# Kernel optimization log

Measured on AMD Instinct MI355X. Metric: run time of the kernel, lower is better.

Reference implementation:

```python
import jax, jax.numpy as jnp
import numpy as np

N_NODES = 100000
N_EDGES = 1600000
N_GRAPHS = 200
NODES_PER_GRAPH = N_NODES // N_GRAPHS
IN_DIM, HID, LAT = 24, 64, 32


def setup_inputs() -> dict:
    key = jax.random.key(0)
    ks = jax.random.split(key, 12)
    x = jax.random.normal(ks[0], (N_NODES, IN_DIM), jnp.float32)
    edge_index = jax.random.randint(ks[1], (2, N_EDGES), 0, N_NODES, jnp.int32)
    batch = (jnp.arange(N_NODES, dtype=jnp.int32) // NODES_PER_GRAPH)
    eps = jax.random.normal(ks[2], (N_GRAPHS, LAT), jnp.float32)

    def lin(k, i, o):
        s = 1.0 / np.sqrt(i)
        return jax.random.uniform(k, (i, o), jnp.float32, -s, s)

    return {
        "x": x, "edge_index": edge_index, "batch": batch, "eps": eps,
        "W1": lin(ks[3], IN_DIM, HID), "b1": jnp.zeros((HID,), jnp.float32),
        "W2": lin(ks[4], HID, HID), "b2": jnp.zeros((HID,), jnp.float32),
        "Wmu": lin(ks[5], HID, LAT), "bmu": jnp.zeros((LAT,), jnp.float32),
        "Wlv": lin(ks[6], HID, LAT), "blv": jnp.zeros((LAT,), jnp.float32),
        "Wd1": lin(ks[7], LAT, 128), "bd1": jnp.zeros((128,), jnp.float32),
        "Wd2": lin(ks[8], 128, IN_DIM), "bd2": jnp.zeros((IN_DIM,), jnp.float32),
        "num_nodes_per_graph": NODES_PER_GRAPH,
        "num_graphs": N_GRAPHS,
    }


def gcn_conv(x, edge_index, W, b, n_nodes):
    # PyG GCNConv: linear transform, add self-loops, symmetric normalization,
    # scatter-add aggregation at target (col) nodes, then bias.
    h = x @ W  # [N, out]
    loops = jnp.arange(n_nodes, dtype=edge_index.dtype)
    row = jnp.concatenate([edge_index[0], loops])  # source nodes
    col = jnp.concatenate([edge_index[1], loops])  # target nodes
    deg = jax.ops.segment_sum(jnp.ones_like(col, h.dtype), col, n_nodes)
    dinv = jnp.where(deg > 0, jax.lax.rsqrt(deg), 0.0)
    norm = dinv[row] * dinv[col]  # [E+N]
    msg = h[row] * norm[:, None]  # gather + scale (memory-bound)
    out = jax.ops.segment_sum(msg, col, n_nodes)  # scatter-add
    return out + b


def reference(x, edge_index, batch, eps, W1, b1, W2, b2, Wmu, bmu, Wlv, blv,
              Wd1, bd1, Wd2, bd2, num_nodes_per_graph, num_graphs):
    n_nodes = x.shape[0]
    h = jax.nn.relu(gcn_conv(x, edge_index, W1, b1, n_nodes))
    h = jax.nn.relu(gcn_conv(h, edge_index, W2, b2, n_nodes))
    # global mean pool over graphs
    sums = jax.ops.segment_sum(h, batch, num_graphs)
    cnt = jax.ops.segment_sum(jnp.ones((n_nodes,), h.dtype), batch, num_graphs)
    pooled = sums / jnp.maximum(cnt, 1.0)[:, None]
    mu = pooled @ Wmu + bmu
    logvar = pooled @ Wlv + blv
    # reparameterize with provided eps (torch.randn_like surrogate)
    z = mu + eps * jnp.exp(0.5 * logvar)
    # decoder: repeat each z num_nodes_per_graph times
    z_exp = jnp.repeat(z, num_nodes_per_graph, axis=0)  # [G*nn, LAT]
    hd = jax.nn.relu(z_exp @ Wd1 + bd1)
    recon_x = jax.nn.sigmoid(hd @ Wd2 + bd2)
    return recon_x, mu, logvar
```

## Files before the change

kernel.cpp:

```cpp
#include <hip/hip_runtime.h>
#include <hip/hip_bf16.h>
#include <hip/hip_fp8.h>

constexpr int N_NODES = 100000;
constexpr int N_EDGES = 1600000;
constexpr int N_GRAPHS = 200;
constexpr int NPG = 500;
constexpr int IN_DIM = 24;
constexpr int HID = 64;
constexpr int LAT = 32;
constexpr int DEC = 128;
constexpr int CAP = 48;
constexpr int P2 = 512;
constexpr int NPP = 196;
constexpr int PART_CAP = 3840;
constexpr int KP_BLOCKS = 200;
constexpr int KP_CHUNK = N_EDGES / KP_BLOCKS;

typedef __attribute__((ext_vector_type(8))) short short8;
typedef __attribute__((ext_vector_type(4))) float f32x4;
typedef __attribute__((ext_vector_type(2))) float f32x2;

constexpr int OFF_CNT = 0;
constexpr int OFF_GCOUNT = 100000;
constexpr int OFF_ROWS = 102400;
constexpr int OFF_A = OFF_ROWS + N_NODES * CAP;
constexpr int OFF_B = OFF_A + N_NODES * HID / 2;
constexpr int OFF_HS1 = OFF_B + N_NODES * HID / 2;
constexpr int OFF_PARTIAL = OFF_HS1 + (N_NODES + 1) * 16;

__global__ __launch_bounds__(1024) void k_part(const int* __restrict__ ei,
                                               int* __restrict__ gcount,
                                               unsigned int* __restrict__ epart) {
    __shared__ int hist[P2];
    __shared__ int ptrs[P2];
    int t = threadIdx.x;
    for (int i = t; i < P2; i += 1024) hist[i] = 0;
    __syncthreads();
    int e0 = blockIdx.x * KP_CHUNK;
    const int4* cols4 = reinterpret_cast<const int4*>(ei + N_EDGES + e0);
    const int4* rows4 = reinterpret_cast<const int4*>(ei + e0);
    for (int i = t; i < KP_CHUNK / 4; i += 1024) {
        int4 c = cols4[i];
        atomicAdd(&hist[c.x / NPP], 1);
        atomicAdd(&hist[c.y / NPP], 1);
        atomicAdd(&hist[c.z / NPP], 1);
        atomicAdd(&hist[c.w / NPP], 1);
    }
    __syncthreads();
    for (int i = t; i < P2; i += 1024) ptrs[i] = atomicAdd(gcount + i, hist[i]);
    __syncthreads();
    for (int i = t; i < KP_CHUNK / 4; i += 1024) {
        int4 c = cols4[i];
        int4 r = rows4[i];
#pragma unroll
        for (int k = 0; k < 4; ++k) {
            int cc = (k == 0) ? c.x : (k == 1) ? c.y : (k == 2) ? c.z : c.w;
            int rr = (k == 0) ? r.x : (k == 1) ? r.y : (k == 2) ? r.z : r.w;
            int p = cc / NPP;
            int cl = cc - p * NPP;
            int pos = atomicAdd(&ptrs[p], 1);
            if (pos < PART_CAP)
                epart[p * PART_CAP + pos] = ((unsigned)cl << 17) | (unsigned)rr;
        }
    }
}

__device__ inline unsigned char f2fp8(float f) {
    __hip_fp8_e4m3 v(f);
    return (unsigned char)v.__x;
}

__device__ inline unsigned short f2bf(float f) {
    __hip_bfloat16 h = __float2bfloat16(f);
    return *reinterpret_cast<unsigned short*>(&h);
}

__global__ __launch_bounds__(256) void k_fill3_lin1(
    const unsigned int* __restrict__ epart, const int* __restrict__ gcount,
    const float* __restrict__ x, const float* __restrict__ W1,
    int* __restrict__ cnt, int* __restrict__ rows,
    unsigned char* __restrict__ HS1) {
    __shared__ int lcnt[NPP];
    __shared__ int lrows[NPP * CAP];
    __shared__ float Ws[IN_DIM * HID];
    int p = blockIdx.x, t = threadIdx.x;
    if (p == 0 && t < 16)
        reinterpret_cast<unsigned int*>(HS1)[N_NODES * 16 + t] = 0;
    for (int i = t; i < NPP; i += 256) lcnt[i] = 0;
    for (int i = t; i < IN_DIM * HID; i += 256) Ws[i] = W1[i];
    __syncthreads();
    int m = min(gcount[p], PART_CAP);
    for (int i = t; i < m; i += 256) {
        unsigned v = epart[p * PART_CAP + i];
        int cl = v >> 17;
        int r = (int)(v & 0x1FFFFu);
        int pos = atomicAdd(&lcnt[cl], 1);
        if (pos < CAP) lrows[cl * CAP + pos] = r;
    }
    __syncthreads();
    for (int i = t; i < NPP; i += 256) {
        int c = min(lcnt[i], CAP);
        int cp = min((c + 3) & ~3, CAP);
        for (int j = c; j < cp; ++j) lrows[i * CAP + j] = N_NODES;
    }
    __syncthreads();
    int node0 = p * NPP;
    int nn = min(NPP, N_NODES - node0);
    if (nn <= 0) return;
    for (int i = t; i < nn * CAP; i += 256) rows[node0 * CAP + i] = lrows[i];
    for (int i = t; i < nn; i += 256) cnt[node0 + i] = lcnt[i];
    __syncthreads();
    float* xs = reinterpret_cast<float*>(lrows);
    for (int i = t; i < nn * IN_DIM; i += 256) xs[i] = x[node0 * IN_DIM + i];
    __syncthreads();
    for (int o = t; o < nn * HID; o += 256) {
        int j = o >> 6, col = o & 63;
        float acc = 0.f;
#pragma unroll
        for (int k = 0; k < IN_DIM; ++k) acc += xs[j * IN_DIM + k] * Ws[k * HID + col];
        float dinv = rsqrtf((float)(lcnt[j] + 1));
        HS1[(node0 + j) * HID + col] = f2fp8(acc * dinv);
    }
}

__device__ inline void acc_fp8x4p(unsigned int u, f32x2& lo, f32x2& hi) {
    lo += __builtin_amdgcn_cvt_pk_f32_fp8(u, false);
    hi += __builtin_amdgcn_cvt_pk_f32_fp8(u, true);
}

__device__ inline void fold4(float4& a) {
    a.x += __shfl_xor(a.x, 16, 64); a.x += __shfl_xor(a.x, 32, 64);
    a.y += __shfl_xor(a.y, 16, 64); a.y += __shfl_xor(a.y, 32, 64);
    a.z += __shfl_xor(a.z, 16, 64); a.z += __shfl_xor(a.z, 32, 64);
    a.w += __shfl_xor(a.w, 16, 64); a.w += __shfl_xor(a.w, 32, 64);
}

__device__ inline void gather_quad(int base, int lane, int np0, int np1,
                                   int np2, int np3,
                                   const int* __restrict__ rows,
                                   const unsigned char* __restrict__ HS,
                                   float4& A0, float4& A1, float4& A2, float4& A3) {
    int fq = lane & 15;
    int rs = lane >> 4;
    const unsigned int* HSq = reinterpret_cast<const unsigned int*>(HS);
    const int* rb = rows + base * CAP;
    int idx0 = (lane < np0) ? rb[lane] : 0;
    int idx1 = (lane < np1) ? rb[CAP + lane] : 0;
    int idx2 = (lane < np2) ? rb[2 * CAP + lane] : 0;
    int idx3 = (lane < np3) ? rb[3 * CAP + lane] : 0;
    f32x2 z = {0.f, 0.f};
    f32x2 l0 = z, h0 = z, l1 = z, h1 = z, l2 = z, h2 = z, l3 = z, h3 = z;
    if (rs == 0)      acc_fp8x4p(HSq[(base + 0) * 16 + fq], l0, h0);
    else if (rs == 1) acc_fp8x4p(HSq[(base + 1) * 16 + fq], l1, h1);
    else if (rs == 2) acc_fp8x4p(HSq[(base + 2) * 16 + fq], l2, h2);
    else              acc_fp8x4p(HSq[(base + 3) * 16 + fq], l3, h3);
    int nw0 = np0 >> 2, nw1 = np1 >> 2, nw2 = np2 >> 2, nw3 = np3 >> 2;
    int gmax = max(max(nw0, nw1), max(nw2, nw3));
    for (int g = 0; g < gmax; g += 4) {
        int m0 = nw0 - g, m1 = nw1 - g, m2 = nw2 - g, m3 = nw3 - g;
        unsigned int u0[4], u1[4], u2[4], u3[4];
#pragma unroll
        for (int k = 0; k < 4; ++k) {
            int sl = 4 * (g + k) + rs;
            if (k < m0) { int r = __shfl(idx0, sl, 64); u0[k] = HSq[r * 16 + fq]; }
            if (k < m1) { int r = __shfl(idx1, sl, 64); u1[k] = HSq[r * 16 + fq]; }
            if (k < m2) { int r = __shfl(idx2, sl, 64); u2[k] = HSq[r * 16 + fq]; }
            if (k < m3) { int r = __shfl(idx3, sl, 64); u3[k] = HSq[r * 16 + fq]; }
        }
#pragma unroll
        for (int k = 0; k < 4; ++k) {
            if (k < m0) acc_fp8x4p(u0[k], l0, h0);
            if (k < m1) acc_fp8x4p(u1[k], l1, h1);
            if (k < m2) acc_fp8x4p(u2[k], l2, h2);
            if (k < m3) acc_fp8x4p(u3[k], l3, h3);
        }
    }
    float4 a0 = {l0.x, l0.y, h0.x, h0.y};
    float4 a1 = {l1.x, l1.y, h1.x, h1.y};
    float4 a2 = {l2.x, l2.y, h2.x, h2.y};
    float4 a3 = {l3.x, l3.y, h3.x, h3.y};
    fold4(a0); fold4(a1); fold4(a2); fold4(a3);
    A0 = a0; A1 = a1; A2 = a2; A3 = a3;
}

__global__ __launch_bounds__(256) void k_gather1(const int* __restrict__ cnt,
                                                 const int* __restrict__ rows,
                                                 const unsigned char* __restrict__ HS1,
                                                 const float* __restrict__ b1,
                                                 unsigned short* __restrict__ H1) {
    int tid = threadIdx.x;
    int w = (blockIdx.x * 256 + tid) >> 6;
    int lane = tid & 63;
    int base = w * 4;
    int cn0 = cnt[base], cn1 = cnt[base + 1], cn2 = cnt[base + 2], cn3 = cnt[base + 3];
    int np0 = (min(cn0, CAP) + 3) & ~3;
    int np1 = (min(cn1, CAP) + 3) & ~3;
    int np2 = (min(cn2, CAP) + 3) & ~3;
    int np3 = (min(cn3, CAP) + 3) & ~3;
    float4 a0, a1, a2, a3;
    gather_quad(base, lane, np0, np1, np2, np3, rows, HS1, a0, a1, a2, a3);
    int fq = lane & 15, rs = lane >> 4;
    float4 bv = reinterpret_cast<const float4*>(b1)[fq];
    float4 a = (rs == 0) ? a0 : (rs == 1) ? a1 : (rs == 2) ? a2 : a3;
    int cn = (rs == 0) ? cn0 : (rs == 1) ? cn1 : (rs == 2) ? cn2 : cn3;
    float dinv = rsqrtf((float)(cn + 1));
    ushort4 o;
    o.x = f2bf(fmaxf(dinv * a.x + bv.x, 0.f));
    o.y = f2bf(fmaxf(dinv * a.y + bv.y, 0.f));
    o.z = f2bf(fmaxf(dinv * a.z + bv.z, 0.f));
    o.w = f2bf(fmaxf(dinv * a.w + bv.w, 0.f));
    *reinterpret_cast<ushort4*>(H1 + (base + rs) * HID + 4 * fq) = o;
}

__global__ __launch_bounds__(256) void k_gemm2(const unsigned short* __restrict__ H1,
                                               const float* __restrict__ W2,
                                               const int* __restrict__ cnt,
                                               unsigned char* __restrict__ HS2) {
    __shared__ unsigned short W2T[HID * 72];
    int tid = threadIdx.x;
    if (blockIdx.x == 0 && tid < 16)
        reinterpret_cast<unsigned int*>(HS2)[N_NODES * 16 + tid] = 0;
    for (int i = tid; i < HID * HID; i += 256) {
        int k = i >> 6, n = i & 63;
        W2T[n * 72 + k] = f2bf(W2[i]);
    }
    __syncthreads();
    int wave = tid >> 6, lane = tid & 63;
    int wid = blockIdx.x * 4 + wave;
    if (wid >= N_NODES / 16) return;
    int row0 = wid * 16;
    int m = lane & 15, quad = lane >> 4;
    const short8* Av = reinterpret_cast<const short8*>(H1);
    short8 a0 = Av[(row0 + m) * 8 + quad];
    short8 a1 = Av[(row0 + m) * 8 + 4 + quad];
    float dv[4];
#pragma unroll
    for (int reg = 0; reg < 4; ++reg)
        dv[reg] = rsqrtf((float)(cnt[row0 + quad * 4 + reg] + 1));
#pragma unroll
    for (int nt = 0; nt < 4; ++nt) {
        short8 b0 = *reinterpret_cast<const short8*>(&W2T[(nt * 16 + m) * 72 + quad * 8]);
        short8 b1 = *reinterpret_cast<const short8*>(&W2T[(nt * 16 + m) * 72 + 32 + quad * 8]);
        f32x4 acc = {0.f, 0.f, 0.f, 0.f};
        acc = __builtin_amdgcn_mfma_f32_16x16x32_bf16(a0, b0, acc, 0, 0, 0);
        acc = __builtin_amdgcn_mfma_f32_16x16x32_bf16(a1, b1, acc, 0, 0, 0);
#pragma unroll
        for (int reg = 0; reg < 4; ++reg) {
            int r = row0 + quad * 4 + reg;
            HS2[r * HID + nt * 16 + m] = f2fp8(acc[reg] * dv[reg]);
        }
    }
}

__global__ __launch_bounds__(256) void k_gather2(const int* __restrict__ cnt,
                                                 const int* __restrict__ rows,
                                                 const unsigned char* __restrict__ HS2,
                                                 const float* __restrict__ b2,
                                                 float* __restrict__ partial) {
    int tid = threadIdx.x;
    int w = (blockIdx.x * 256 + tid) >> 6;
    int lane = tid & 63;
    int base = w * 4;
    int cn0 = cnt[base], cn1 = cnt[base + 1], cn2 = cnt[base + 2], cn3 = cnt[base + 3];
    int np0 = (min(cn0, CAP) + 3) & ~3;
    int np1 = (min(cn1, CAP) + 3) & ~3;
    int np2 = (min(cn2, CAP) + 3) & ~3;
    int np3 = (min(cn3, CAP) + 3) & ~3;
    float4 a0, a1, a2, a3;
    gather_quad(base, lane, np0, np1, np2, np3, rows, HS2, a0, a1, a2, a3);
    int fq = lane & 15, rs = lane >> 4;
    float4 bv = reinterpret_cast<const float4*>(b2)[fq];
    float d0 = rsqrtf((float)(cn0 + 1));
    float d1 = rsqrtf((float)(cn1 + 1));
    float d2 = rsqrtf((float)(cn2 + 1));
    float d3 = rsqrtf((float)(cn3 + 1));
    float4 s;
    s.x = fmaxf(d0 * a0.x + bv.x, 0.f) + fmaxf(d1 * a1.x + bv.x, 0.f) +
          fmaxf(d2 * a2.x + bv.x, 0.f) + fmaxf(d3 * a3.x + bv.x, 0.f);
    s.y = fmaxf(d0 * a0.y + bv.y, 0.f) + fmaxf(d1 * a1.y + bv.y, 0.f) +
          fmaxf(d2 * a2.y + bv.y, 0.f) + fmaxf(d3 * a3.y + bv.y, 0.f);
    s.z = fmaxf(d0 * a0.z + bv.z, 0.f) + fmaxf(d1 * a1.z + bv.z, 0.f) +
          fmaxf(d2 * a2.z + bv.z, 0.f) + fmaxf(d3 * a3.z + bv.z, 0.f);
    s.w = fmaxf(d0 * a0.w + bv.w, 0.f) + fmaxf(d1 * a1.w + bv.w, 0.f) +
          fmaxf(d2 * a2.w + bv.w, 0.f) + fmaxf(d3 * a3.w + bv.w, 0.f);
    if (rs == 0) reinterpret_cast<float4*>(partial + w * HID)[fq] = s;
}

__global__ __launch_bounds__(128) void k_head_bcast(
    const float* __restrict__ partial, const float* __restrict__ eps,
    const float* __restrict__ Wmu, const float* __restrict__ bmu,
    const float* __restrict__ Wlv, const float* __restrict__ blv,
    const float* __restrict__ Wd1, const float* __restrict__ bd1,
    const float* __restrict__ Wd2, const float* __restrict__ bd2,
    float* __restrict__ out_mu, float* __restrict__ out_lv,
    float* __restrict__ out_recon) {
    int g = blockIdx.x, tid = threadIdx.x;
    __shared__ float p[HID];
    __shared__ float zs[LAT];
    __shared__ float hds[DEC];
    __shared__ __align__(16) float rg[IN_DIM];
    if (tid < HID) {
        float s = 0.f;
#pragma unroll 5
        for (int r = 0; r < NPG / 4; ++r)
            s += partial[(g * (NPG / 4) + r) * HID + tid];
        p[tid] = s * (1.0f / NPG);
    }
    __syncthreads();
    if (tid < LAT) {
        float m = bmu[tid], l = blv[tid];
#pragma unroll 8
        for (int k = 0; k < HID; ++k) {
            m += p[k] * Wmu[k * LAT + tid];
            l += p[k] * Wlv[k * LAT + tid];
        }
        out_mu[g * LAT + tid] = m;
        out_lv[g * LAT + tid] = l;
        zs[tid] = m + eps[g * LAT + tid] * expf(0.5f * l);
    }
    __syncthreads();
    {
        float a = bd1[tid];
#pragma unroll 8
        for (int k = 0; k < LAT; ++k) a += zs[k] * Wd1[k * DEC + tid];
        hds[tid] = fmaxf(a, 0.f);
    }
    __syncthreads();
    if (tid < IN_DIM) {
        float a = bd2[tid];
#pragma unroll 8
        for (int k = 0; k < DEC; ++k) a += hds[k] * Wd2[k * IN_DIM + tid];
        rg[tid] = 1.0f / (1.0f + expf(-a));
    }
    __syncthreads();
    const float4* rg4 = reinterpret_cast<const float4*>(rg);
    float4* dst = reinterpret_cast<float4*>(out_recon + g * NPG * IN_DIM);
    for (int j = tid; j < NPG * IN_DIM / 4; j += 128) dst[j] = rg4[j % (IN_DIM / 4)];
}

extern "C" void kernel_launch(void* const* d_in, const int* in_sizes, int n_in,
                              void* d_out, int out_size, void* d_ws, size_t ws_size,
                              hipStream_t stream) {
    const float* x = (const float*)d_in[0];
    const int* ei = (const int*)d_in[1];
    const float* eps = (const float*)d_in[3];
    const float* W1 = (const float*)d_in[4];
    const float* b1 = (const float*)d_in[5];
    const float* W2 = (const float*)d_in[6];
    const float* b2 = (const float*)d_in[7];
    const float* Wmu = (const float*)d_in[8];
    const float* bmu = (const float*)d_in[9];
    const float* Wlv = (const float*)d_in[10];
    const float* blv = (const float*)d_in[11];
    const float* Wd1 = (const float*)d_in[12];
    const float* bd1 = (const float*)d_in[13];
    const float* Wd2 = (const float*)d_in[14];
    const float* bd2 = (const float*)d_in[15];

    float* ws = (float*)d_ws;
    int* cnt = (int*)ws + OFF_CNT;
    int* gcount = (int*)ws + OFF_GCOUNT;
    int* rows = (int*)ws + OFF_ROWS;
    unsigned int* epart = (unsigned int*)((int*)ws + OFF_A);
    unsigned char* HS1 = (unsigned char*)((int*)ws + OFF_HS1);
    unsigned short* H1 = (unsigned short*)((int*)ws + OFF_B);
    unsigned char* HS2 = (unsigned char*)((int*)ws + OFF_A);
    float* partial = ws + OFF_PARTIAL;

    float* out = (float*)d_out;
    float* out_recon = out;
    float* out_mu = out + N_NODES * IN_DIM;
    float* out_lv = out_mu + N_GRAPHS * LAT;

    hipMemsetAsync(gcount, 0, P2 * sizeof(int), stream);

    k_part<<<KP_BLOCKS, 1024, 0, stream>>>(ei, gcount, epart);
    k_fill3_lin1<<<P2, 256, 0, stream>>>(epart, gcount, x, W1, cnt, rows, HS1);

    k_gather1<<<N_NODES / 16, 256, 0, stream>>>(cnt, rows, HS1, b1, H1);
    k_gemm2<<<(N_NODES / 16 + 3) / 4, 256, 0, stream>>>(H1, W2, cnt, HS2);

    k_gather2<<<N_NODES / 16, 256, 0, stream>>>(cnt, rows, HS2, b2, partial);

    k_head_bcast<<<N_GRAPHS, 128, 0, stream>>>(partial, eps, Wmu, bmu, Wlv, blv,
                                               Wd1, bd1, Wd2, bd2, out_mu,
                                               out_lv, out_recon);
}
```

Measured before the change: 246.3 us.

## Fuse layer-1 gather with layer-2 MFMA GEMM and remap gather to node-per-quarter-wave

Merges the layer-1 neighbour gather and the W2 bf16 MFMA transform into one kernel, so H1 is staged in shared memory instead of being written to and re-read from global memory, and one launch is removed. The gather is restructured so that each 16-lane group of a wave handles one node with a fixed unrolled batch of 32 (optionally 48) neighbour loads, with invalid slots pointing at the zero sentinel row. This drops the padding pass in the fill kernel. The fixed unroll trades wasted loads on low-degree nodes for more memory-level parallelism. Every gather block now also converts W2 into shared memory, and nontemporal loads and stores are used for the index and partial data.

Measured after the change: 205.4 us. 1.2x faster.

```diff
diff --git a/kernel.cpp b/kernel.cpp
--- a/kernel.cpp
+++ b/kernel.cpp
@@ -99,12 +99,6 @@
         if (pos < CAP) lrows[cl * CAP + pos] = r;
     }
     __syncthreads();
-    for (int i = t; i < NPP; i += 256) {
-        int c = min(lcnt[i], CAP);
-        int cp = min((c + 3) & ~3, CAP);
-        for (int j = c; j < cp; ++j) lrows[i * CAP + j] = N_NODES;
-    }
-    __syncthreads();
     int node0 = p * NPP;
     int nn = min(NPP, N_NODES - node0);
     if (nn <= 0) return;
@@ -129,95 +123,62 @@
     hi += __builtin_amdgcn_cvt_pk_f32_fp8(u, true);
 }
 
-__device__ inline void fold4(float4& a) {
-    a.x += __shfl_xor(a.x, 16, 64); a.x += __shfl_xor(a.x, 32, 64);
-    a.y += __shfl_xor(a.y, 16, 64); a.y += __shfl_xor(a.y, 32, 64);
-    a.z += __shfl_xor(a.z, 16, 64); a.z += __shfl_xor(a.z, 32, 64);
-    a.w += __shfl_xor(a.w, 16, 64); a.w += __shfl_xor(a.w, 32, 64);
-}
-
-__device__ inline void gather_quad(int base, int lane, int np0, int np1,
-                                   int np2, int np3,
-                                   const int* __restrict__ rows,
-                                   const unsigned char* __restrict__ HS,
-                                   float4& A0, float4& A1, float4& A2, float4& A3) {
-    int fq = lane & 15;
-    int rs = lane >> 4;
+__device__ inline void gatherT(int base, int lane,
+                               const int* __restrict__ cnt,
+                               const int* __restrict__ rows,
+                               const unsigned char* __restrict__ HS,
+                               f32x2& lo, f32x2& hi, int& cn_out) {
+    int fq = lane & 15, rs = lane >> 4;
     const unsigned int* HSq = reinterpret_cast<const unsigned int*>(HS);
-    const int* rb = rows + base * CAP;
-    int idx0 = (lane < np0) ? rb[lane] : 0;
-    int idx1 = (lane < np1) ? rb[CAP + lane] : 0;
-    int idx2 = (lane < np2) ? rb[2 * CAP + lane] : 0;
-    int idx3 = (lane < np3) ? rb[3 * CAP + lane] : 0;
+    int node = base + rs;
+    int cn = __builtin_nontemporal_load(cnt + node);
+    int np = min(cn, CAP);
+    int mx = np;
+    mx = max(mx, __shfl_xor(mx, 16, 64));
+    mx = max(mx, __shfl_xor(mx, 32, 64));
+    const int* rb = rows + node * CAP;
+    int idx0 = (fq < np)      ? __builtin_nontemporal_load(rb + fq)      : N_NODES;
+    int idx1 = (16 + fq < np) ? __builtin_nontemporal_load(rb + 16 + fq) : N_NODES;
+    int idx2 = (32 + fq < np) ? __builtin_nontemporal_load(rb + 32 + fq) : N_NODES;
     f32x2 z = {0.f, 0.f};
-    f32x2 l0 = z, h0 = z, l1 = z, h1 = z, l2 = z, h2 = z, l3 = z, h3 = z;
-    if (rs == 0)      acc_fp8x4p(HSq[(base + 0) * 16 + fq], l0, h0);
-    else if (rs == 1) acc_fp8x4p(HSq[(base + 1) * 16 + fq], l1, h1);
-    else if (rs == 2) acc_fp8x4p(HSq[(base + 2) * 16 + fq], l2, h2);
-    else              acc_fp8x4p(HSq[(base + 3) * 16 + fq], l3, h3);
-    int nw0 = np0 >> 2, nw1 = np1 >> 2, nw2 = np2 >> 2, nw3 = np3 >> 2;
-    int gmax = max(max(nw0, nw1), max(nw2, nw3));
-    for (int g = 0; g < gmax; g += 4) {
-        int m0 = nw0 - g, m1 = nw1 - g, m2 = nw2 - g, m3 = nw3 - g;
-        unsigned int u0[4], u1[4], u2[4], u3[4];
-#pragma unroll
-        for (int k = 0; k < 4; ++k) {
-            int sl = 4 * (g + k) + rs;
-            if (k < m0) { int r = __shfl(idx0, sl, 64); u0[k] = HSq[r * 16 + fq]; }
-            if (k < m1) { int r = __shfl(idx1, sl, 64); u1[k] = HSq[r * 16 + fq]; }
-            if (k < m2) { int r = __shfl(idx2, sl, 64); u2[k] = HSq[r * 16 + fq]; }
-            if (k < m3) { int r = __shfl(idx3, sl, 64); u3[k] = HSq[r * 16 + fq]; }
-        }
-#pragma unroll
-        for (int k = 0; k < 4; ++k) {
-            if (k < m0) acc_fp8x4p(u0[k], l0, h0);
-            if (k < m1) acc_fp8x4p(u1[k], l1, h1);
-            if (k < m2) acc_fp8x4p(u2[k], l2, h2);
-            if (k < m3) acc_fp8x4p(u3[k], l3, h3);
-        }
-    }
-    float4 a0 = {l0.x, l0.y, h0.x, h0.y};
-    float4 a1 = {l1.x, l1.y, h1.x, h1.y};
-    float4 a2 = {l2.x, l2.y, h2.x, h2.y};
-    float4 a3 = {l3.x, l3.y, h3.x, h3.y};
-    fold4(a0); fold4(a1); fold4(a2); fold4(a3);
-    A0 = a0; A1 = a1; A2 = a2; A3 = a3;
-}
-
-__global__ __launch_bounds__(256) void k_gather1(const int* __restrict__ cnt,
-                                                 const int* __restrict__ rows,
-                                                 const unsigned char* __restrict__ HS1,
-                                                 const float* __restrict__ b1,
-                                                 unsigned short* __restrict__ H1) {
-    int tid = threadIdx.x;
-    int w = (blockIdx.x * 256 + tid) >> 6;
-    int lane = tid & 63;
-    int base = w * 4;
-    int cn0 = cnt[base], cn1 = cnt[base + 1], cn2 = cnt[base + 2], cn3 = cnt[base + 3];
-    int np0 = (min(cn0, CAP) + 3) & ~3;
-    int np1 = (min(cn1, CAP) + 3) & ~3;
-    int np2 = (min(cn2, CAP) + 3) & ~3;
-    int np3 = (min(cn3, CAP) + 3) & ~3;
-    float4 a0, a1, a2, a3;
-    gather_quad(base, lane, np0, np1, np2, np3, rows, HS1, a0, a1, a2, a3);
-    int fq = lane & 15, rs = lane >> 4;
-    float4 bv = reinterpret_cast<const float4*>(b1)[fq];
-    float4 a = (rs == 0) ? a0 : (rs == 1) ? a1 : (rs == 2) ? a2 : a3;
-    int cn = (rs == 0) ? cn0 : (rs == 1) ? cn1 : (rs == 2) ? cn2 : cn3;
-    float dinv = rsqrtf((float)(cn + 1));
-    ushort4 o;
-    o.x = f2bf(fmaxf(dinv * a.x + bv.x, 0.f));
-    o.y = f2bf(fmaxf(dinv * a.y + bv.y, 0.f));
-    o.z = f2bf(fmaxf(dinv * a.z + bv.z, 0.f));
-    o.w = f2bf(fmaxf(dinv * a.w + bv.w, 0.f));
-    *reinterpret_cast<ushort4*>(H1 + (base + rs) * HID + 4 * fq) = o;
-}
-
-__global__ __launch_bounds__(256) void k_gemm2(const unsigned short* __restrict__ H1,
-                                               const float* __restrict__ W2,
-                                               const int* __restrict__ cnt,
-                                               unsigned char* __restrict__ HS2) {
+    lo = z; hi = z;
+    acc_fp8x4p(HSq[node * 16 + fq], lo, hi);
+    int rbase = rs * 16;
+    {
+        unsigned int u[32];
+#pragma unroll
+        for (int c = 0; c < 16; ++c) {
+            int r = __shfl(idx0, rbase + c, 64);
+            u[c] = HSq[r * 16 + fq];
+        }
+#pragma unroll
+        for (int c = 0; c < 16; ++c) {
+            int r = __shfl(idx1, rbase + c, 64);
+            u[16 + c] = HSq[r * 16 + fq];
+        }
+#pragma unroll
+        for (int c = 0; c < 32; ++c) acc_fp8x4p(u[c], lo, hi);
+    }
+    if (mx > 32) {
+        unsigned int u[16];
+#pragma unroll
+        for (int c = 0; c < 16; ++c) {
+            int r = __shfl(idx2, rbase + c, 64);
+            u[c] = HSq[r * 16 + fq];
+        }
+#pragma unroll
+        for (int c = 0; c < 16; ++c) acc_fp8x4p(u[c], lo, hi);
+    }
+    cn_out = cn;
+}
+
+__global__ __launch_bounds__(256) void k_gather1mm(
+    const int* __restrict__ cnt, const int* __restrict__ rows,
+    const unsigned char* __restrict__ HS1, const float* __restrict__ b1,
+    const float* __restrict__ W2, unsigned char* __restrict__ HS2) {
     __shared__ unsigned short W2T[HID * 72];
+    __shared__ unsigned short H1s[16 * 72];
+    __shared__ float dinvL[16];
     int tid = threadIdx.x;
     if (blockIdx.x == 0 && tid < 16)
         reinterpret_cast<unsigned int*>(HS2)[N_NODES * 16 + tid] = 0;
@@ -225,31 +186,36 @@
         int k = i >> 6, n = i & 63;
         W2T[n * 72 + k] = f2bf(W2[i]);
     }
-    __syncthreads();
     int wave = tid >> 6, lane = tid & 63;
-    int wid = blockIdx.x * 4 + wave;
-    if (wid >= N_NODES / 16) return;
-    int row0 = wid * 16;
+    int fq = lane & 15, rs = lane >> 4;
+    int base = blockIdx.x * 16 + wave * 4;
+    f32x2 lo, hi;
+    int cn;
+    gatherT(base, lane, cnt, rows, HS1, lo, hi, cn);
+    float dinv = rsqrtf((float)(cn + 1));
+    float4 bv = reinterpret_cast<const float4*>(b1)[fq];
+    int r = wave * 4 + rs;
+    ushort4 o;
+    o.x = f2bf(fmaxf(dinv * lo.x + bv.x, 0.f));
+    o.y = f2bf(fmaxf(dinv * lo.y + bv.y, 0.f));
+    o.z = f2bf(fmaxf(dinv * hi.x + bv.z, 0.f));
+    o.w = f2bf(fmaxf(dinv * hi.y + bv.w, 0.f));
+    *reinterpret_cast<ushort4*>(&H1s[r * 72 + fq * 4]) = o;
+    if (fq == 0) dinvL[r] = dinv;
+    __syncthreads();
     int m = lane & 15, quad = lane >> 4;
-    const short8* Av = reinterpret_cast<const short8*>(H1);
-    short8 a0 = Av[(row0 + m) * 8 + quad];
-    short8 a1 = Av[(row0 + m) * 8 + 4 + quad];
-    float dv[4];
-#pragma unroll
-    for (int reg = 0; reg < 4; ++reg)
-        dv[reg] = rsqrtf((float)(cnt[row0 + quad * 4 + reg] + 1));
-#pragma unroll
-    for (int nt = 0; nt < 4; ++nt) {
-        short8 b0 = *reinterpret_cast<const short8*>(&W2T[(nt * 16 + m) * 72 + quad * 8]);
-        short8 b1 = *reinterpret_cast<const short8*>(&W2T[(nt * 16 + m) * 72 + 32 + quad * 8]);
-        f32x4 acc = {0.f, 0.f, 0.f, 0.f};
-        acc = __builtin_amdgcn_mfma_f32_16x16x32_bf16(a0, b0, acc, 0, 0, 0);
-        acc = __builtin_amdgcn_mfma_f32_16x16x32_bf16(a1, b1, acc, 0, 0, 0);
-#pragma unroll
-        for (int reg = 0; reg < 4; ++reg) {
-            int r = row0 + quad * 4 + reg;
-            HS2[r * HID + nt * 16 + m] = f2fp8(acc[reg] * dv[reg]);
-        }
+    short8 a0 = *reinterpret_cast<const short8*>(&H1s[m * 72 + quad * 8]);
+    short8 a1 = *reinterpret_cast<const short8*>(&H1s[m * 72 + 32 + quad * 8]);
+    short8 b0 = *reinterpret_cast<const short8*>(&W2T[(wave * 16 + m) * 72 + quad * 8]);
+    short8 b1v = *reinterpret_cast<const short8*>(&W2T[(wave * 16 + m) * 72 + 32 + quad * 8]);
+    f32x4 acc = {0.f, 0.f, 0.f, 0.f};
+    acc = __builtin_amdgcn_mfma_f32_16x16x32_bf16(a0, b0, acc, 0, 0, 0);
+    acc = __builtin_amdgcn_mfma_f32_16x16x32_bf16(a1, b1v, acc, 0, 0, 0);
+    int row0 = blockIdx.x * 16;
+#pragma unroll
+    for (int reg = 0; reg < 4; ++reg) {
+        int rr = quad * 4 + reg;
+        HS2[(row0 + rr) * HID + wave * 16 + m] = f2fp8(acc[reg] * dinvL[rr]);
     }
 }
 
@@ -259,32 +225,26 @@
                                                  const float* __restrict__ b2,
                                                  float* __restrict__ partial) {
     int tid = threadIdx.x;
-    int w = (blockIdx.x * 256 + tid) >> 6;
-    int lane = tid & 63;
+    int wave = tid >> 6, lane = tid & 63;
+    int w = blockIdx.x * 4 + wave;
     int base = w * 4;
-    int cn0 = cnt[base], cn1 = cnt[base + 1], cn2 = cnt[base + 2], cn3 = cnt[base + 3];
-    int np0 = (min(cn0, CAP) + 3) & ~3;
-    int np1 = (min(cn1, CAP) + 3) & ~3;
-    int np2 = (min(cn2, CAP) + 3) & ~3;
-    int np3 = (min(cn3, CAP) + 3) & ~3;
-    float4 a0, a1, a2, a3;
-    gather_quad(base, lane, np0, np1, np2, np3, rows, HS2, a0, a1, a2, a3);
+    f32x2 lo, hi;
+    int cn;
+    gatherT(base, lane, cnt, rows, HS2, lo, hi, cn);
     int fq = lane & 15, rs = lane >> 4;
+    float dinv = rsqrtf((float)(cn + 1));
     float4 bv = reinterpret_cast<const float4*>(b2)[fq];
-    float d0 = rsqrtf((float)(cn0 + 1));
-    float d1 = rsqrtf((float)(cn1 + 1));
-    float d2 = rsqrtf((float)(cn2 + 1));
-    float d3 = rsqrtf((float)(cn3 + 1));
-    float4 s;
-    s.x = fmaxf(d0 * a0.x + bv.x, 0.f) + fmaxf(d1 * a1.x + bv.x, 0.f) +
-          fmaxf(d2 * a2.x + bv.x, 0.f) + fmaxf(d3 * a3.x + bv.x, 0.f);
-    s.y = fmaxf(d0 * a0.y + bv.y, 0.f) + fmaxf(d1 * a1.y + bv.y, 0.f) +
-          fmaxf(d2 * a2.y + bv.y, 0.f) + fmaxf(d3 * a3.y + bv.y, 0.f);
-    s.z = fmaxf(d0 * a0.z + bv.z, 0.f) + fmaxf(d1 * a1.z + bv.z, 0.f) +
-          fmaxf(d2 * a2.z + bv.z, 0.f) + fmaxf(d3 * a3.z + bv.z, 0.f);
-    s.w = fmaxf(d0 * a0.w + bv.w, 0.f) + fmaxf(d1 * a1.w + bv.w, 0.f) +
-          fmaxf(d2 * a2.w + bv.w, 0.f) + fmaxf(d3 * a3.w + bv.w, 0.f);
-    if (rs == 0) reinterpret_cast<float4*>(partial + w * HID)[fq] = s;
+    f32x4 h;
+    h.x = fmaxf(dinv * lo.x + bv.x, 0.f);
+    h.y = fmaxf(dinv * lo.y + bv.y, 0.f);
+    h.z = fmaxf(dinv * hi.x + bv.z, 0.f);
+    h.w = fmaxf(dinv * hi.y + bv.w, 0.f);
+    h.x += __shfl_xor(h.x, 16, 64); h.x += __shfl_xor(h.x, 32, 64);
+    h.y += __shfl_xor(h.y, 16, 64); h.y += __shfl_xor(h.y, 32, 64);
+    h.z += __shfl_xor(h.z, 16, 64); h.z += __shfl_xor(h.z, 32, 64);
+    h.w += __shfl_xor(h.w, 16, 64); h.w += __shfl_xor(h.w, 32, 64);
+    if (rs == 0)
+        __builtin_nontemporal_store(h, reinterpret_cast<f32x4*>(partial + w * HID) + fq);
 }
 
 __global__ __launch_bounds__(128) void k_head_bcast(
@@ -364,7 +324,6 @@
     int* rows = (int*)ws + OFF_ROWS;
     unsigned int* epart = (unsigned int*)((int*)ws + OFF_A);
     unsigned char* HS1 = (unsigned char*)((int*)ws + OFF_HS1);
-    unsigned short* H1 = (unsigned short*)((int*)ws + OFF_B);
     unsigned char* HS2 = (unsigned char*)((int*)ws + OFF_A);
     float* partial = ws + OFF_PARTIAL;
 
@@ -378,8 +337,7 @@
     k_part<<<KP_BLOCKS, 1024, 0, stream>>>(ei, gcount, epart);
     k_fill3_lin1<<<P2, 256, 0, stream>>>(epart, gcount, x, W1, cnt, rows, HS1);
 
-    k_gather1<<<N_NODES / 16, 256, 0, stream>>>(cnt, rows, HS1, b1, H1);
-    k_gemm2<<<(N_NODES / 16 + 3) / 4, 256, 0, stream>>>(H1, W2, cnt, HS2);
+    k_gather1mm<<<N_NODES / 16, 256, 0, stream>>>(cnt, rows, HS1, b1, W2, HS2);
 
     k_gather2<<<N_NODES / 16, 256, 0, stream>>>(cnt, rows, HS2, b2, partial);
 
```
